# Kernel tuning notes

Measured on AMD Instinct MI355X. Metric: run time of the kernel, lower is better.

Reference implementation:

```python
import jax, jax.numpy as jnp
import numpy as np
from jax import lax

B_, L_ = 2, 512
D_MODEL, EXPAND, HEAD_DIM, NGROUPS, D_STATE, D_CONV = 512, 2, 64, 1, 64, 3
D_INNER = EXPAND * D_MODEL            # 1024
NHEADS = D_INNER // HEAD_DIM          # 16
CONV_DIM = D_INNER + 2 * NGROUPS * D_STATE   # 1152
D_IN_PROJ = 2 * D_INNER + 2 * NGROUPS * D_STATE + NHEADS  # 2192
RMS_EPS = 1e-5


def silu(x):
    return x * jax.nn.sigmoid(x)


def segsum(x):
    # x: (..., T) -> (..., T, T); out[..., i, j] = sum_{j<k<=i} x[..., k], -inf above diag
    T = x.shape[-1]
    xr = jnp.broadcast_to(x[..., None], x.shape + (T,))
    keep = jnp.tril(jnp.ones((T, T), dtype=bool), -1)
    xr = jnp.where(keep, xr, 0.0)
    s = jnp.cumsum(xr, axis=-2)
    diag = jnp.tril(jnp.ones((T, T), dtype=bool), 0)
    return jnp.where(diag, s, -jnp.inf)


def ssd(x, A, Bm, Cm, chunk):
    # x: (b,l,h,p), A: (b,l,h), Bm/Cm: (b,l,g,n); chunk==1 as in the source forward
    b, l, h, p = x.shape
    c = l // chunk
    n = Bm.shape[-1]
    x = x.reshape(b, c, chunk, h, p)
    Bm = Bm.reshape(b, c, chunk, Bm.shape[2], n)
    Cm = Cm.reshape(b, c, chunk, Cm.shape[2], n)
    A = A.reshape(b, c, chunk, h).transpose(0, 3, 1, 2)        # (b,h,c,l)
    A_cumsum = jnp.cumsum(A, axis=-1)
    Lmat = jnp.exp(segsum(A))                                   # (b,h,c,l,l)
    # broadcast group dim (g==1) to heads, matching torch.einsum broadcasting
    Bb = jnp.broadcast_to(Bm, (b, c, chunk, h, n))
    Cb = jnp.broadcast_to(Cm, (b, c, chunk, h, n))
    Y_diag = jnp.einsum('bclhn,bcshn,bhcls,bcshp->bclhp', Cb, Bb, Lmat, x)
    decay_states = jnp.exp(A_cumsum[:, :, :, -1:] - A_cumsum)   # (b,h,c,l)
    states = jnp.einsum('bclhn,bhcl,bclhp->bchpn', Bb, decay_states, x)
    states = jnp.concatenate([jnp.zeros_like(states[:, :1]), states], axis=1)  # (b,c+1,h,p,n)
    A_last = jnp.pad(A_cumsum[:, :, :, -1], ((0, 0), (0, 0), (1, 0)))          # (b,h,c+1)
    decay_chunk = jnp.exp(segsum(A_last))                       # (b,h,c+1,c+1)
    new_states = jnp.einsum('bhzc,bchpn->bzhpn', decay_chunk, states)
    states = new_states[:, :-1]                                 # (b,c,h,p,n)
    state_decay_out = jnp.exp(A_cumsum)
    Y_off = jnp.einsum('bclhn,bchpn,bhcl->bclhp', Cb, states, state_decay_out)
    return (Y_diag + Y_off).reshape(b, l, h, p)


def causal_dwconv(x, w, bias):
    # x: (B,L,C); w: (C,K) depthwise; torch pads (K-1) both sides then slices [:L] == left-pad only
    xt = x.transpose(0, 2, 1)
    y = lax.conv_general_dilated(xt, w[:, None, :], (1,), [(D_CONV - 1, 0)],
                                 feature_group_count=CONV_DIM,
                                 dimension_numbers=('NCH', 'OIH', 'NCH'))
    return y.transpose(0, 2, 1) + bias


def setup_inputs() -> dict:
    key = jax.random.key(0)
    ks = jax.random.split(key, 8)
    u = jax.random.normal(ks[0], (B_, L_, D_MODEL), dtype=jnp.float32)
    W_in = jax.random.normal(ks[1], (D_MODEL, D_IN_PROJ), dtype=jnp.float32) / np.sqrt(D_MODEL).astype(np.float32)
    conv_w = jax.random.normal(ks[2], (CONV_DIM, D_CONV), dtype=jnp.float32) * 0.3
    conv_b = jnp.zeros((CONV_DIM,), dtype=jnp.float32)
    dt = jnp.exp(jax.random.uniform(ks[3], (NHEADS,), dtype=jnp.float32)
                 * (np.float32(np.log(0.1)) - np.float32(np.log(0.001))) + np.float32(np.log(0.001)))
    dt = jnp.clip(dt, 1e-4, None)
    dt_bias = dt + jnp.log(-jnp.expm1(-dt))
    A_log = jnp.log(jax.random.uniform(ks[4], (NHEADS,), dtype=jnp.float32, minval=1.0, maxval=16.0))
    D_param = jnp.ones((NHEADS,), dtype=jnp.float32)
    rms_w = jnp.ones((D_INNER,), dtype=jnp.float32)
    W_out = jax.random.normal(ks[5], (D_INNER, D_MODEL), dtype=jnp.float32) / np.sqrt(D_INNER).astype(np.float32)
    return {"u": u, "W_in": W_in, "conv_w": conv_w, "conv_b": conv_b, "dt_bias": dt_bias,
            "A_log": A_log, "D_param": D_param, "rms_w": rms_w, "W_out": W_out}


def reference(u, W_in, conv_w, conv_b, dt_bias, A_log, D_param, rms_w, W_out):
    b, l, _ = u.shape
    zxbcdt = u @ W_in                                   # (b,l,D_IN_PROJ)
    z = zxbcdt[..., :D_INNER]
    xBC = zxbcdt[..., D_INNER:D_INNER + CONV_DIM]
    dt = zxbcdt[..., D_INNER + CONV_DIM:]
    dt = jax.nn.softplus(dt + dt_bias)                  # (b,l,h)
    A = -jnp.exp(A_log)                                 # (h,)
    xBC = silu(causal_dwconv(xBC, conv_w, conv_b))      # (b,l,CONV_DIM)
    x = xBC[..., :D_INNER].reshape(b, l, NHEADS, HEAD_DIM)
    Bm = xBC[..., D_INNER:D_INNER + D_STATE][:, :, None, :]     # (b,l,1,n)
    Cm = xBC[..., D_INNER + D_STATE:][:, :, None, :]            # (b,l,1,n)
    y = ssd(x * dt[..., None], A * dt, Bm, Cm, 1)       # (b,l,h,p)
    y = y + x * D_param[:, None]
    y = y.reshape(b, l, D_INNER)
    # gated RMSNorm
    yz = y * silu(z)
    y = yz * lax.rsqrt(jnp.mean(yz * yz, axis=-1, keepdims=True) + RMS_EPS) * rms_w
    return y @ W_out
```

## Files before the change

### kernel.cpp

```cpp
#include <hip/hip_runtime.h>
#include <hip/hip_bf16.h>

#define B_SZ 2
#define L_SZ 512
#define D_MODEL 512
#define D_INNER 1024
#define HEAD_DIM 64
#define NHEADS 16
#define D_STATE 64
#define D_CONV 3
#define CONV_DIM 1152
#define D_IN_PROJ 2192
#define BL (B_SZ * L_SZ)
#define RMS_EPS 1e-5f
#define QC 64
#define NCH 8
#define NPAD1 2304
#define PB 72

typedef __attribute__((ext_vector_type(8))) short short8t;
typedef __attribute__((ext_vector_type(8))) unsigned short ushort8t;
typedef __attribute__((ext_vector_type(4))) unsigned short ushort4t;
typedef __attribute__((ext_vector_type(4))) float f32x4;

__device__ __forceinline__ unsigned short f2bf(float f) {
    unsigned u = __float_as_uint(f);
    u += 0x7fff + ((u >> 16) & 1);
    return (unsigned short)(u >> 16);
}
__device__ __forceinline__ float bf2f(unsigned short u) {
    return __uint_as_float(((unsigned)u) << 16);
}

__device__ __forceinline__ void gload_lds16(const void* g, void* lds) {
    __builtin_amdgcn_global_load_lds(
        (const __attribute__((address_space(1))) unsigned int*)g,
        (__attribute__((address_space(3))) unsigned int*)lds, 16, 0, 0);
}

__device__ __forceinline__ void transpose_tile_bf16(const float* __restrict__ src,
                                                    unsigned short* __restrict__ dst,
                                                    int K, int Nin, int tile, int ntn) {
    __shared__ float T[64][65];
    int tid = threadIdx.x;
    int nt = tile % ntn, kt = tile / ntn;
    int n0 = nt * 64, k0 = kt * 64;
#pragma unroll
    for (int rr = 0; rr < 4; ++rr) {
        int k = k0 + (tid >> 4) + rr * 16;
        int nn = (tid & 15) * 4;
#pragma unroll
        for (int q = 0; q < 4; ++q) {
            int n = n0 + nn + q;
            T[(tid >> 4) + rr * 16][nn + q] = (n < Nin) ? src[(size_t)k * Nin + n] : 0.f;
        }
    }
    __syncthreads();
    int nn2 = tid >> 2, kc = tid & 3;
    unsigned short ov[16];
#pragma unroll
    for (int j = 0; j < 16; ++j) ov[j] = f2bf(T[kc * 16 + j][nn2]);
    unsigned short* p = dst + (size_t)(n0 + nn2) * K + k0 + kc * 16;
    *(ushort8t*)p = *(ushort8t*)&ov[0];
    *(ushort8t*)(p + 8) = *(ushort8t*)&ov[8];
}

__global__ __launch_bounds__(256) void prep_kernel(const float* __restrict__ W_in,
                                                   const float* __restrict__ W_out,
                                                   const float* __restrict__ u,
                                                   unsigned short* __restrict__ Wt1,
                                                   unsigned short* __restrict__ Wt2,
                                                   unsigned short* __restrict__ u_bf) {
    int bid = blockIdx.x;
    if (bid < 288) {
        transpose_tile_bf16(W_in, Wt1, D_MODEL, D_IN_PROJ, bid, 36);
    } else if (bid < 416) {
        transpose_tile_bf16(W_out, Wt2, D_INNER, D_MODEL, bid - 288, 8);
    } else {
        int i = ((bid - 416) * 256 + threadIdx.x) * 8;
        float4 v0 = *(const float4*)(u + i);
        float4 v1 = *(const float4*)(u + i + 4);
        unsigned short ov[8] = {f2bf(v0.x), f2bf(v0.y), f2bf(v0.z), f2bf(v0.w),
                                f2bf(v1.x), f2bf(v1.y), f2bf(v1.z), f2bf(v1.w)};
        *(ushort8t*)(u_bf + i) = *(ushort8t*)&ov[0];
    }
}

__global__ __launch_bounds__(256) void gemm_in(const unsigned short* __restrict__ A,
                                               const unsigned short* __restrict__ Bt,
                                               float* __restrict__ C,
                                               unsigned short* __restrict__ xbc,
                                               float* __restrict__ dtb) {
    const int K = D_MODEL;
    __shared__ char sm[49152];
    int tid = threadIdx.x;
    int w = tid >> 6, l = tid & 63;
    int m0 = blockIdx.y * 64, n0 = blockIdx.x * 64;
    int wm = w >> 1, wn = w & 1;

    f32x4 acc[2][2];
#pragma unroll
    for (int i = 0; i < 2; ++i)
#pragma unroll
        for (int j = 0; j < 2; ++j) acc[i][j] = (f32x4){0.f, 0.f, 0.f, 0.f};

    auto stage = [&](const unsigned short* src, int row0, int k0, char* dst) {
#pragma unroll
        for (int p = 0; p < 2; ++p) {
            int c = w * 2 + p;
            int row = c * 8 + (l >> 3);
            int scb = ((l & 7) << 4) ^ ((row & 7) << 4);
            gload_lds16(src + (size_t)(row0 + row) * K + k0 + (scb >> 1), dst + c * 1024);
        }
    };

    const int nkt = K / 64;
    stage(A, m0, 0, sm);
    stage(Bt, n0, 0, sm + 8192);
    stage(A, m0, 64, sm + 16384);
    stage(Bt, n0, 64, sm + 16384 + 8192);

    for (int kt = 0; kt < nkt; ++kt) {
        if (kt + 2 < nkt) {
            char* d = sm + ((kt + 2) % 3) * 16384;
            stage(A, m0, (kt + 2) * 64, d);
            stage(Bt, n0, (kt + 2) * 64, d + 8192);
        }
        int inflight = nkt - 1 - kt;
        if (inflight >= 2)      asm volatile("s_waitcnt vmcnt(8)" ::: "memory");
        else if (inflight == 1) asm volatile("s_waitcnt vmcnt(4)" ::: "memory");
        else                    asm volatile("s_waitcnt vmcnt(0)" ::: "memory");
        __builtin_amdgcn_s_barrier();

        const char* Ab = sm + (kt % 3) * 16384;
        const char* Bb = Ab + 8192;
#pragma unroll
        for (int kk = 0; kk < 2; ++kk) {
            short8t af[2], bf[2];
#pragma unroll
            for (int i = 0; i < 2; ++i) {
                int r = wm * 32 + i * 16 + (l & 15);
                int cb = (kk * 64 + (l >> 4) * 16) ^ ((r & 7) << 4);
                af[i] = *(const short8t*)(Ab + r * 128 + cb);
            }
#pragma unroll
            for (int j = 0; j < 2; ++j) {
                int r = wn * 32 + j * 16 + (l & 15);
                int cb = (kk * 64 + (l >> 4) * 16) ^ ((r & 7) << 4);
                bf[j] = *(const short8t*)(Bb + r * 128 + cb);
            }
#pragma unroll
            for (int i = 0; i < 2; ++i)
#pragma unroll
                for (int j = 0; j < 2; ++j)
                    acc[i][j] = __builtin_amdgcn_mfma_f32_16x16x32_bf16(af[i], bf[j], acc[i][j], 0, 0, 0);
        }
        __builtin_amdgcn_s_barrier();
    }

#pragma unroll
    for (int i = 0; i < 2; ++i)
#pragma unroll
        for (int j = 0; j < 2; ++j) {
            int row = m0 + wm * 32 + i * 16 + (l >> 4) * 4;
            int col = n0 + wn * 32 + j * 16 + (l & 15);
#pragma unroll
            for (int r = 0; r < 4; ++r) {
                float v = acc[i][j][r];
                int rr = row + r;
                if (col < D_INNER) {
                    C[(size_t)rr * D_IN_PROJ + col] = v;
                } else if (col < D_INNER + CONV_DIM) {
                    xbc[(size_t)rr * CONV_DIM + (col - D_INNER)] = f2bf(v);
                } else if (col < D_IN_PROJ) {
                    dtb[(size_t)rr * 16 + (col - D_INNER - CONV_DIM)] = v;
                }
            }
        }
}

__global__ __launch_bounds__(256) void gemm_mfma32(const unsigned short* __restrict__ A,
                                                   const unsigned short* __restrict__ Bt,
                                                   float* __restrict__ C,
                                                   int N, int K) {
    __shared__ char sm[36864];
    int tid = threadIdx.x;
    int w = tid >> 6, l = tid & 63;
    int m0 = blockIdx.y * 32, n0 = blockIdx.x * 64;
    int wm = w >> 1, wn = w & 1;

    f32x4 acc[2];
    acc[0] = (f32x4){0.f, 0.f, 0.f, 0.f};
    acc[1] = (f32x4){0.f, 0.f, 0.f, 0.f};

    auto stageA = [&](int k0, char* dst) {
        int row = w * 8 + (l >> 3);
        int scb = ((l & 7) << 4) ^ ((row & 7) << 4);
        gload_lds16(A + (size_t)(m0 + row) * K + k0 + (scb >> 1), dst + w * 1024);
    };
    auto stageB = [&](int k0, char* dst) {
#pragma unroll
        for (int p = 0; p < 2; ++p) {
            int c = w * 2 + p;
            int row = c * 8 + (l >> 3);
            int scb = ((l & 7) << 4) ^ ((row & 7) << 4);
            gload_lds16(Bt + (size_t)(n0 + row) * K + k0 + (scb >> 1), dst + c * 1024);
        }
    };

    int nkt = K / 64;
    stageA(0, sm); stageB(0, sm + 4096);
    stageA(64, sm + 12288); stageB(64, sm + 12288 + 4096);

    for (int kt = 0; kt < nkt; ++kt) {
        if (kt + 2 < nkt) {
            char* d = sm + ((kt + 2) % 3) * 12288;
            stageA((kt + 2) * 64, d);
            stageB((kt + 2) * 64, d + 4096);
        }
        int inflight = nkt - 1 - kt;
        if (inflight >= 2)      asm volatile("s_waitcnt vmcnt(6)" ::: "memory");
        else if (inflight == 1) asm volatile("s_waitcnt vmcnt(3)" ::: "memory");
        else                    asm volatile("s_waitcnt vmcnt(0)" ::: "memory");
        __builtin_amdgcn_s_barrier();

        const char* Ab = sm + (kt % 3) * 12288;
        const char* Bb = Ab + 4096;
#pragma unroll
        for (int kk = 0; kk < 2; ++kk) {
            short8t af;
            {
                int r = wm * 16 + (l & 15);
                int cb = (kk * 64 + (l >> 4) * 16) ^ ((r & 7) << 4);
                af = *(const short8t*)(Ab + r * 128 + cb);
            }
#pragma unroll
            for (int j = 0; j < 2; ++j) {
                int r = wn * 32 + j * 16 + (l & 15);
                int cb = (kk * 64 + (l >> 4) * 16) ^ ((r & 7) << 4);
                short8t bfv = *(const short8t*)(Bb + r * 128 + cb);
                acc[j] = __builtin_amdgcn_mfma_f32_16x16x32_bf16(af, bfv, acc[j], 0, 0, 0);
            }
        }
        __builtin_amdgcn_s_barrier();
    }

#pragma unroll
    for (int j = 0; j < 2; ++j) {
        int col = n0 + wn * 32 + j * 16 + (l & 15);
        int rowb = m0 + wm * 16 + (l >> 4) * 4;
#pragma unroll
        for (int r = 0; r < 4; ++r)
            C[(size_t)(rowb + r) * N + col] = acc[j][r];
    }
}

__device__ __forceinline__ float4 conv4b(const unsigned short* __restrict__ xrow,
                                         int gl, int ch,
                                         const float* __restrict__ conv_w,
                                         const float* __restrict__ conv_b) {
    ushort4t u2 = *(const ushort4t*)(xrow + ch);
    ushort4t u1 = {0, 0, 0, 0}, u0 = {0, 0, 0, 0};
    if (gl >= 1) u1 = *(const ushort4t*)(xrow + ch - CONV_DIM);
    if (gl >= 2) u0 = *(const ushort4t*)(xrow + ch - 2 * CONV_DIM);
    float4 o;
    float a;
    a = conv_b[ch+0] + conv_w[(ch+0)*3]*bf2f(u0[0]) + conv_w[(ch+0)*3+1]*bf2f(u1[0]) + conv_w[(ch+0)*3+2]*bf2f(u2[0]);
    o.x = a / (1.f + __expf(-a));
    a = conv_b[ch+1] + conv_w[(ch+1)*3]*bf2f(u0[1]) + conv_w[(ch+1)*3+1]*bf2f(u1[1]) + conv_w[(ch+1)*3+2]*bf2f(u2[1]);
    o.y = a / (1.f + __expf(-a));
    a = conv_b[ch+2] + conv_w[(ch+2)*3]*bf2f(u0[2]) + conv_w[(ch+2)*3+1]*bf2f(u1[2]) + conv_w[(ch+2)*3+2]*bf2f(u2[2]);
    o.z = a / (1.f + __expf(-a));
    a = conv_b[ch+3] + conv_w[(ch+3)*3]*bf2f(u0[3]) + conv_w[(ch+3)*3+1]*bf2f(u1[3]) + conv_w[(ch+3)*3+2]*bf2f(u2[3]);
    o.w = a / (1.f + __expf(-a));
    return o;
}

__global__ __launch_bounds__(256) void ssd_passA(const unsigned short* __restrict__ xbc,
                                                 const float* __restrict__ dtb,
                                                 const float* __restrict__ conv_w,
                                                 const float* __restrict__ conv_b,
                                                 const float* __restrict__ dt_bias,
                                                 const float* __restrict__ A_log,
                                                 const float* __restrict__ D_param,
                                                 float* __restrict__ y,
                                                 float* __restrict__ Zbuf,
                                                 float* __restrict__ Ebuf) {
    int blk = blockIdx.x;
    int h = blk & 15;
    int c = (blk >> 4) & 7;
    int b = blk >> 7;
    int tid = threadIdx.x;

    __shared__ __align__(16) unsigned short Cs_bf[QC][PB];
    __shared__ __align__(16) unsigned short Bs_bf[QC][PB];
    __shared__ __align__(16) unsigned short XDT_bf[QC][PB];
    __shared__ __align__(16) unsigned short BTw_bf[QC][PB];
    __shared__ float csh[QC], dts[QC], wh[QC];
#define PS_bf Cs_bf

    int bl0 = b * L_SZ + c * QC;

    if (tid < 64) {
        int t = tid;
        float draw = dtb[(size_t)(bl0 + t) * 16 + h];
        float dtv = draw + dt_bias[h];
        dtv = (dtv > 20.f) ? dtv : log1pf(expf(dtv));
        float A = -expf(A_log[h]);
        float cs = A * dtv;
#pragma unroll
        for (int off = 1; off < 64; off <<= 1) {
            float tmp = __shfl_up(cs, off);
            if (t >= off) cs += tmp;
        }
        float cs63 = __shfl(cs, 63);
        dts[t] = dtv;
        csh[t] = cs;
        wh[t] = __expf(cs63 - cs);
        Ebuf[(((size_t)(b * NHEADS + h) * NCH) + c) * QC + t] = __expf(cs);
    }

    int row16 = tid >> 4;
    int col4 = (tid & 15) * 4;
#pragma unroll
    for (int r = 0; r < 4; ++r) {
        int t = r * 16 + row16;
        int gl = c * QC + t;
        const unsigned short* xrow = xbc + (size_t)(bl0 + t) * CONV_DIM;
        float4 Bv = conv4b(xrow, gl, D_INNER + col4, conv_w, conv_b);
        float4 Cv = conv4b(xrow, gl, D_INNER + D_STATE + col4, conv_w, conv_b);
        ushort4t bq = {f2bf(Bv.x), f2bf(Bv.y), f2bf(Bv.z), f2bf(Bv.w)};
        ushort4t cq = {f2bf(Cv.x), f2bf(Cv.y), f2bf(Cv.z), f2bf(Cv.w)};
        *(ushort4t*)&Bs_bf[t][col4] = bq;
        *(ushort4t*)&Cs_bf[t][col4] = cq;
    }
    __syncthreads();

#pragma unroll
    for (int r = 0; r < 4; ++r) {
        int t = r * 16 + row16;
        int gl = c * QC + t;
        const unsigned short* xrow = xbc + (size_t)(bl0 + t) * CONV_DIM;
        float4 xv = conv4b(xrow, gl, h * HEAD_DIM + col4, conv_w, conv_b);
        float d = dts[t], wt = wh[t];
        xv.x *= d; xv.y *= d; xv.z *= d; xv.w *= d;
        ushort4t xq = {f2bf(xv.x), f2bf(xv.y), f2bf(xv.z), f2bf(xv.w)};
        ushort4t bq = *(ushort4t*)&Bs_bf[t][col4];
#pragma unroll
        for (int q = 0; q < 4; ++q) {
            XDT_bf[col4 + q][t] = xq[q];
            BTw_bf[col4 + q][t] = f2bf(bf2f(bq[q]) * wt);
        }
    }
    __syncthreads();

    int l = tid & 63, wv = tid >> 6;
    int wm = wv >> 1, wn = wv & 1;
    int fr = l & 15, fq = l >> 4;

    f32x4 g[2][2];
    {
#pragma unroll
        for (int i = 0; i < 2; ++i)
#pragma unroll
            for (int j = 0; j < 2; ++j) g[i][j] = (f32x4){0.f, 0.f, 0.f, 0.f};
#pragma unroll
        for (int kk = 0; kk < 2; ++kk) {
            short8t af[2], bb[2];
#pragma unroll
            for (int i = 0; i < 2; ++i)
                af[i] = *(const short8t*)&Cs_bf[wm * 32 + i * 16 + fr][kk * 32 + fq * 8];
#pragma unroll
            for (int j = 0; j < 2; ++j)
                bb[j] = *(const short8t*)&Bs_bf[wn * 32 + j * 16 + fr][kk * 32 + fq * 8];
#pragma unroll
            for (int i = 0; i < 2; ++i)
#pragma unroll
                for (int j = 0; j < 2; ++j)
                    g[i][j] = __builtin_amdgcn_mfma_f32_16x16x32_bf16(af[i], bb[j], g[i][j], 0, 0, 0);
        }
    }
    __syncthreads();

    {
#pragma unroll
        for (int i = 0; i < 2; ++i)
#pragma unroll
            for (int j = 0; j < 2; ++j) {
                int s = wn * 32 + j * 16 + fr;
                float css = csh[s];
#pragma unroll
                for (int r = 0; r < 4; ++r) {
                    int t = wm * 32 + i * 16 + fq * 4 + r;
                    float v = (s <= t) ? g[i][j][r] * __expf(csh[t] - css) : 0.f;
                    PS_bf[t][s] = f2bf(v);
                }
            }
    }
    __syncthreads();

    {
        f32x4 yv[2][2];
#pragma unroll
        for (int i = 0; i < 2; ++i)
#pragma unroll
            for (int j = 0; j < 2; ++j) yv[i][j] = (f32x4){0.f, 0.f, 0.f, 0.f};
#pragma unroll
        for (int kk = 0; kk < 2; ++kk) {
            short8t af[2], bb[2];
#pragma unroll
            for (int i = 0; i < 2; ++i)
                af[i] = *(const short8t*)&PS_bf[wm * 32 + i * 16 + fr][kk * 32 + fq * 8];
#pragma unroll
            for (int j = 0; j < 2; ++j)
                bb[j] = *(const short8t*)&XDT_bf[wn * 32 + j * 16 + fr][kk * 32 + fq * 8];
#pragma unroll
            for (int i = 0; i < 2; ++i)
#pragma unroll
                for (int j = 0; j < 2; ++j)
                    yv[i][j] = __builtin_amdgcn_mfma_f32_16x16x32_bf16(af[i], bb[j], yv[i][j], 0, 0, 0);
        }
        float Dp = D_param[h];
#pragma unroll
        for (int i = 0; i < 2; ++i)
#pragma unroll
            for (int j = 0; j < 2; ++j) {
                int p = wn * 32 + j * 16 + fr;
#pragma unroll
                for (int r = 0; r < 4; ++r) {
                    int t = wm * 32 + i * 16 + fq * 4 + r;
                    float xval = bf2f(XDT_bf[p][t]);
                    float fct = Dp / dts[t];
                    y[(size_t)(bl0 + t) * D_INNER + h * HEAD_DIM + p] =
                        yv[i][j][r] + fct * xval;
                }
            }
    }

    {
        f32x4 zv[2][2];
#pragma unroll
        for (int i = 0; i < 2; ++i)
#pragma unroll
            for (int j = 0; j < 2; ++j) zv[i][j] = (f32x4){0.f, 0.f, 0.f, 0.f};
#pragma unroll
        for (int kk = 0; kk < 2; ++kk) {
            short8t af[2], bb[2];
#pragma unroll
            for (int i = 0; i < 2; ++i)
                af[i] = *(const short8t*)&XDT_bf[wm * 32 + i * 16 + fr][kk * 32 + fq * 8];
#pragma unroll
            for (int j = 0; j < 2; ++j)
                bb[j] = *(const short8t*)&BTw_bf[wn * 32 + j * 16 + fr][kk * 32 + fq * 8];
#pragma unroll
            for (int i = 0; i < 2; ++i)
#pragma unroll
                for (int j = 0; j < 2; ++j)
                    zv[i][j] = __builtin_amdgcn_mfma_f32_16x16x32_bf16(af[i], bb[j], zv[i][j], 0, 0, 0);
        }
        float* Zr = Zbuf + (((size_t)(b * NHEADS + h) * NCH) + c) * (HEAD_DIM * D_STATE);
#pragma unroll
        for (int i = 0; i < 2; ++i)
#pragma unroll
            for (int j = 0; j < 2; ++j) {
                int n = wn * 32 + j * 16 + fr;
#pragma unroll
                for (int r = 0; r < 4; ++r) {
                    int p = wm * 32 + i * 16 + fq * 4 + r;
                    Zr[p * D_STATE + n] = zv[i][j][r];
                }
            }
    }
#undef PS_bf
}

__global__ __launch_bounds__(256) void ssd_passC(const unsigned short* __restrict__ xbc,
                                                 const float* __restrict__ conv_w,
                                                 const float* __restrict__ conv_b,
                                                 const float* __restrict__ Zbuf,
                                                 const float* __restrict__ Ebuf,
                                                 float* __restrict__ y) {
    int blk = blockIdx.x;
    int h = blk & 15;
    int q = blk >> 4;
    int c = 1 + (q % 7);
    int b = q / 7;
    int tid = threadIdx.x;

    __shared__ __align__(16) unsigned short Cs_bf[QC][PB];
    __shared__ __align__(16) unsigned short S_bf[QC][PB];
    __shared__ float Eh[QC];

    int bl0 = b * L_SZ + c * QC;
    const float* Zb = Zbuf + ((size_t)(b * NHEADS + h) * NCH) * (HEAD_DIM * D_STATE);
    const float* Eb = Ebuf + ((size_t)(b * NHEADS + h) * NCH) * QC;

    {
        int p = tid >> 2, nq = (tid & 3) * 16;
        float S16[16];
#pragma unroll
        for (int qq = 0; qq < 16; ++qq) S16[qq] = 0.f;
        float wgt = 1.f;
        for (int j = c - 1; j >= 0; --j) {
            const float* Zj = Zb + (size_t)j * (HEAD_DIM * D_STATE) + p * D_STATE + nq;
#pragma unroll
            for (int q4 = 0; q4 < 4; ++q4) {
                float4 z = *(const float4*)(Zj + q4 * 4);
                S16[q4 * 4 + 0] += wgt * z.x;
                S16[q4 * 4 + 1] += wgt * z.y;
                S16[q4 * 4 + 2] += wgt * z.z;
                S16[q4 * 4 + 3] += wgt * z.w;
            }
            wgt *= Eb[(size_t)j * QC + 63];
        }
#pragma unroll
        for (int q4 = 0; q4 < 4; ++q4) {
            ushort4t s4 = {f2bf(S16[q4 * 4 + 0]), f2bf(S16[q4 * 4 + 1]),
                           f2bf(S16[q4 * 4 + 2]), f2bf(S16[q4 * 4 + 3])};
            *(ushort4t*)&S_bf[p][nq + q4 * 4] = s4;
        }
    }

    int row16 = tid >> 4, col4 = (tid & 15) * 4;
#pragma unroll
    for (int r = 0; r < 4; ++r) {
        int t = r * 16 + row16;
        int gl = c * QC + t;
        const unsigned short* xrow = xbc + (size_t)(bl0 + t) * CONV_DIM;
        float4 Cv = conv4b(xrow, gl, D_INNER + D_STATE + col4, conv_w, conv_b);
        ushort4t cq = {f2bf(Cv.x), f2bf(Cv.y), f2bf(Cv.z), f2bf(Cv.w)};
        *(ushort4t*)&Cs_bf[t][col4] = cq;
    }
    if (tid < 64)
        Eh[tid] = Ebuf[(((size_t)(b * NHEADS + h) * NCH) + c) * QC + tid];
    __syncthreads();

    int l = tid & 63, wv = tid >> 6;
    int wm = wv >> 1, wn = wv & 1;
    int fr = l & 15, fq = l >> 4;
    f32x4 acc[2][2];
#pragma unroll
    for (int i = 0; i < 2; ++i)
#pragma unroll
        for (int j = 0; j < 2; ++j) acc[i][j] = (f32x4){0.f, 0.f, 0.f, 0.f};
#pragma unroll
    for (int kk = 0; kk < 2; ++kk) {
        short8t af[2], bb[2];
#pragma unroll
        for (int i = 0; i < 2; ++i)
            af[i] = *(const short8t*)&Cs_bf[wm * 32 + i * 16 + fr][kk * 32 + fq * 8];
#pragma unroll
        for (int j = 0; j < 2; ++j)
            bb[j] = *(const short8t*)&S_bf[wn * 32 + j * 16 + fr][kk * 32 + fq * 8];
#pragma unroll
        for (int i = 0; i < 2; ++i)
#pragma unroll
            for (int j = 0; j < 2; ++j)
                acc[i][j] = __builtin_amdgcn_mfma_f32_16x16x32_bf16(af[i], bb[j], acc[i][j], 0, 0, 0);
    }
#pragma unroll
    for (int i = 0; i < 2; ++i)
#pragma unroll
        for (int j = 0; j < 2; ++j) {
            int p = wn * 32 + j * 16 + fr;
#pragma unroll
            for (int r = 0; r < 4; ++r) {
                int t = wm * 32 + i * 16 + fq * 4 + r;
                float* yp = y + (size_t)(bl0 + t) * D_INNER + h * HEAD_DIM + p;
                *yp += Eh[t] * acc[i][j][r];
            }
        }
}

__global__ __launch_bounds__(256) void gated_rmsnorm_kernel(const float* __restrict__ zxbcdt,
                                                            const float* __restrict__ y,
                                                            const float* __restrict__ rms_w,
                                                            unsigned short* __restrict__ yn_bf) {
    int bl = blockIdx.x;
    int tid = threadIdx.x;
    __shared__ float red[4];
    __shared__ float sscale;
    float vals[4];
    float sumsq = 0.f;
#pragma unroll
    for (int i = 0; i < 4; ++i) {
        int col = tid + i * 256;
        float yv = y[(size_t)bl * D_INNER + col];
        float z = zxbcdt[(size_t)bl * D_IN_PROJ + col];
        float yz = yv * (z / (1.f + expf(-z)));
        vals[i] = yz;
        sumsq += yz * yz;
    }
#pragma unroll
    for (int off = 32; off; off >>= 1) sumsq += __shfl_xor(sumsq, off);
    int wave = tid >> 6, lane = tid & 63;
    if (lane == 0) red[wave] = sumsq;
    __syncthreads();
    if (tid == 0) {
        float t = red[0] + red[1] + red[2] + red[3];
        sscale = rsqrtf(t / (float)D_INNER + RMS_EPS);
    }
    __syncthreads();
    float sc = sscale;
#pragma unroll
    for (int i = 0; i < 4; ++i) {
        int col = tid + i * 256;
        yn_bf[(size_t)bl * D_INNER + col] = f2bf(vals[i] * sc * rms_w[col]);
    }
}

extern "C" void kernel_launch(void* const* d_in, const int* in_sizes, int n_in,
                              void* d_out, int out_size, void* d_ws, size_t ws_size,
                              hipStream_t stream) {
    const float* u       = (const float*)d_in[0];
    const float* W_in    = (const float*)d_in[1];
    const float* conv_w  = (const float*)d_in[2];
    const float* conv_b  = (const float*)d_in[3];
    const float* dt_bias = (const float*)d_in[4];
    const float* A_log   = (const float*)d_in[5];
    const float* D_param = (const float*)d_in[6];
    const float* rms_w   = (const float*)d_in[7];
    const float* W_out   = (const float*)d_in[8];
    float* out = (float*)d_out;

    float* ws = (float*)d_ws;
    float* zxbcdt = ws;
    float* y      = zxbcdt + (size_t)BL * D_IN_PROJ;
    float* Zbuf   = y + (size_t)BL * D_INNER;
    float* Ebuf   = Zbuf + (size_t)32 * NCH * 4096;
    float* dtb    = Ebuf + (size_t)32 * NCH * QC;
    unsigned short* u_bf  = (unsigned short*)(dtb + (size_t)BL * 16);
    unsigned short* Wt1   = u_bf + (size_t)BL * D_MODEL;
    unsigned short* Wt2   = Wt1 + (size_t)NPAD1 * D_MODEL;
    unsigned short* yn_bf = Wt2 + (size_t)D_MODEL * D_INNER;
    unsigned short* xbc   = yn_bf + (size_t)BL * D_INNER;

    prep_kernel<<<672, 256, 0, stream>>>(W_in, W_out, u, Wt1, Wt2, u_bf);

    gemm_in<<<dim3(NPAD1 / 64, BL / 64), 256, 0, stream>>>(
        u_bf, Wt1, zxbcdt, xbc, dtb);

    ssd_passA<<<B_SZ * NCH * NHEADS, 256, 0, stream>>>(
        xbc, dtb, conv_w, conv_b, dt_bias, A_log, D_param, y, Zbuf, Ebuf);
    ssd_passC<<<224, 256, 0, stream>>>(
        xbc, conv_w, conv_b, Zbuf, Ebuf, y);

    gated_rmsnorm_kernel<<<BL, 256, 0, stream>>>(zxbcdt, y, rms_w, yn_bf);

    gemm_mfma32<<<dim3(D_MODEL / 64, BL / 32), 256, 0, stream>>>(
        yn_bf, Wt2, out, D_MODEL, D_INNER);
}
```

Measured before the change: 46.97 us.

## Hoist conv+SiLU and softplus into a separate kernel; stage SSD tiles via LDS DMA

Moves the causal depthwise conv, SiLU and dt softplus out of the SSD chunk kernels into a dedicated per-row kernel that writes bf16 activations once. The chunk kernels then load B, C and X tiles with direct global-to-LDS loads into swizzled layouts, and XOR-swizzled transposed buffers replace the padded ones. This removes the conv work that was repeated for B and C across 16 heads and for C in pass C. The cost is an extra launch and an extra round trip of the conv output through global memory.

```diff
diff --git a/kernel.cpp b/kernel.cpp
--- a/kernel.cpp
+++ b/kernel.cpp
@@ -16,7 +16,6 @@
 #define QC 64
 #define NCH 8
 #define NPAD1 2304
-#define PB 72
 
 typedef __attribute__((ext_vector_type(8))) short short8t;
 typedef __attribute__((ext_vector_type(8))) unsigned short ushort8t;
@@ -177,82 +176,6 @@
                 }
             }
         }
-}
-
-__global__ __launch_bounds__(256) void gemm_mfma32(const unsigned short* __restrict__ A,
-                                                   const unsigned short* __restrict__ Bt,
-                                                   float* __restrict__ C,
-                                                   int N, int K) {
-    __shared__ char sm[36864];
-    int tid = threadIdx.x;
-    int w = tid >> 6, l = tid & 63;
-    int m0 = blockIdx.y * 32, n0 = blockIdx.x * 64;
-    int wm = w >> 1, wn = w & 1;
-
-    f32x4 acc[2];
-    acc[0] = (f32x4){0.f, 0.f, 0.f, 0.f};
-    acc[1] = (f32x4){0.f, 0.f, 0.f, 0.f};
-
-    auto stageA = [&](int k0, char* dst) {
-        int row = w * 8 + (l >> 3);
-        int scb = ((l & 7) << 4) ^ ((row & 7) << 4);
-        gload_lds16(A + (size_t)(m0 + row) * K + k0 + (scb >> 1), dst + w * 1024);
-    };
-    auto stageB = [&](int k0, char* dst) {
-#pragma unroll
-        for (int p = 0; p < 2; ++p) {
-            int c = w * 2 + p;
-            int row = c * 8 + (l >> 3);
-            int scb = ((l & 7) << 4) ^ ((row & 7) << 4);
-            gload_lds16(Bt + (size_t)(n0 + row) * K + k0 + (scb >> 1), dst + c * 1024);
-        }
-    };
-
-    int nkt = K / 64;
-    stageA(0, sm); stageB(0, sm + 4096);
-    stageA(64, sm + 12288); stageB(64, sm + 12288 + 4096);
-
-    for (int kt = 0; kt < nkt; ++kt) {
-        if (kt + 2 < nkt) {
-            char* d = sm + ((kt + 2) % 3) * 12288;
-            stageA((kt + 2) * 64, d);
-            stageB((kt + 2) * 64, d + 4096);
-        }
-        int inflight = nkt - 1 - kt;
-        if (inflight >= 2)      asm volatile("s_waitcnt vmcnt(6)" ::: "memory");
-        else if (inflight == 1) asm volatile("s_waitcnt vmcnt(3)" ::: "memory");
-        else                    asm volatile("s_waitcnt vmcnt(0)" ::: "memory");
-        __builtin_amdgcn_s_barrier();
-
-        const char* Ab = sm + (kt % 3) * 12288;
-        const char* Bb = Ab + 4096;
-#pragma unroll
-        for (int kk = 0; kk < 2; ++kk) {
-            short8t af;
-            {
-                int r = wm * 16 + (l & 15);
-                int cb = (kk * 64 + (l >> 4) * 16) ^ ((r & 7) << 4);
-                af = *(const short8t*)(Ab + r * 128 + cb);
-            }
-#pragma unroll
-            for (int j = 0; j < 2; ++j) {
-                int r = wn * 32 + j * 16 + (l & 15);
-                int cb = (kk * 64 + (l >> 4) * 16) ^ ((r & 7) << 4);
-                short8t bfv = *(const short8t*)(Bb + r * 128 + cb);
-                acc[j] = __builtin_amdgcn_mfma_f32_16x16x32_bf16(af, bfv, acc[j], 0, 0, 0);
-            }
-        }
-        __builtin_amdgcn_s_barrier();
-    }
-
-#pragma unroll
-    for (int j = 0; j < 2; ++j) {
-        int col = n0 + wn * 32 + j * 16 + (l & 15);
-        int rowb = m0 + wm * 16 + (l >> 4) * 4;
-#pragma unroll
-        for (int r = 0; r < 4; ++r)
-            C[(size_t)(rowb + r) * N + col] = acc[j][r];
-    }
 }
 
 __device__ __forceinline__ float4 conv4b(const unsigned short* __restrict__ xrow,
@@ -276,11 +199,30 @@
     return o;
 }
 
-__global__ __launch_bounds__(256) void ssd_passA(const unsigned short* __restrict__ xbc,
-                                                 const float* __restrict__ dtb,
-                                                 const float* __restrict__ conv_w,
-                                                 const float* __restrict__ conv_b,
-                                                 const float* __restrict__ dt_bias,
+__global__ __launch_bounds__(256) void conv_silu_kernel(const unsigned short* __restrict__ xbc,
+                                                        const float* __restrict__ conv_w,
+                                                        const float* __restrict__ conv_b,
+                                                        const float* __restrict__ dtb,
+                                                        const float* __restrict__ dt_bias,
+                                                        unsigned short* __restrict__ xc,
+                                                        float* __restrict__ dtp) {
+    int bl = blockIdx.x;
+    int gl = bl & (L_SZ - 1);
+    int tid = threadIdx.x;
+    const unsigned short* xrow = xbc + (size_t)bl * CONV_DIM;
+    for (int ch = tid * 4; ch < CONV_DIM; ch += 1024) {
+        float4 o = conv4b(xrow, gl, ch, conv_w, conv_b);
+        ushort4t q = {f2bf(o.x), f2bf(o.y), f2bf(o.z), f2bf(o.w)};
+        *(ushort4t*)(xc + (size_t)bl * CONV_DIM + ch) = q;
+    }
+    if (tid < 16) {
+        float d = dtb[(size_t)bl * 16 + tid] + dt_bias[tid];
+        dtp[(size_t)bl * 16 + tid] = (d > 20.f) ? d : log1pf(expf(d));
+    }
+}
+
+__global__ __launch_bounds__(256) void ssd_passA(const unsigned short* __restrict__ xc,
+                                                 const float* __restrict__ dtp,
                                                  const float* __restrict__ A_log,
                                                  const float* __restrict__ D_param,
                                                  float* __restrict__ y,
@@ -291,21 +233,35 @@
     int c = (blk >> 4) & 7;
     int b = blk >> 7;
     int tid = threadIdx.x;
-
-    __shared__ __align__(16) unsigned short Cs_bf[QC][PB];
-    __shared__ __align__(16) unsigned short Bs_bf[QC][PB];
-    __shared__ __align__(16) unsigned short XDT_bf[QC][PB];
-    __shared__ __align__(16) unsigned short BTw_bf[QC][PB];
+    int w = tid >> 6, l = tid & 63;
+
+    __shared__ __align__(16) unsigned short Bs[64 * 64];
+    __shared__ __align__(16) unsigned short Cs[64 * 64];
+    __shared__ __align__(16) unsigned short Xs[64 * 64];
+    __shared__ __align__(16) unsigned short XDT[64 * 72];
+    __shared__ __align__(16) unsigned short BTw[64 * 72];
+    __shared__ __align__(16) unsigned short P[64 * 72];
     __shared__ float csh[QC], dts[QC], wh[QC];
-#define PS_bf Cs_bf
 
     int bl0 = b * L_SZ + c * QC;
+    const unsigned short* xbase = xc + (size_t)bl0 * CONV_DIM;
+
+    auto stageT = [&](const unsigned short* src, unsigned short* dst) {
+#pragma unroll
+        for (int p = 0; p < 2; ++p) {
+            int cc = w * 2 + p;
+            int row = cc * 8 + (l >> 3);
+            int scb = ((l & 7) << 4) ^ ((row & 7) << 4);
+            gload_lds16(src + (size_t)row * CONV_DIM + (scb >> 1), (char*)dst + cc * 1024);
+        }
+    };
+    stageT(xbase + D_INNER, Bs);
+    stageT(xbase + D_INNER + D_STATE, Cs);
+    stageT(xbase + h * HEAD_DIM, Xs);
 
     if (tid < 64) {
         int t = tid;
-        float draw = dtb[(size_t)(bl0 + t) * 16 + h];
-        float dtv = draw + dt_bias[h];
-        dtv = (dtv > 20.f) ? dtv : log1pf(expf(dtv));
+        float dtv = dtp[(size_t)(bl0 + t) * 16 + h];
         float A = -expf(A_log[h]);
         float cs = A * dtv;
 #pragma unroll
@@ -319,43 +275,29 @@
         wh[t] = __expf(cs63 - cs);
         Ebuf[(((size_t)(b * NHEADS + h) * NCH) + c) * QC + t] = __expf(cs);
     }
+    asm volatile("s_waitcnt vmcnt(0)" ::: "memory");
+    __syncthreads();
 
     int row16 = tid >> 4;
     int col4 = (tid & 15) * 4;
 #pragma unroll
     for (int r = 0; r < 4; ++r) {
         int t = r * 16 + row16;
-        int gl = c * QC + t;
-        const unsigned short* xrow = xbc + (size_t)(bl0 + t) * CONV_DIM;
-        float4 Bv = conv4b(xrow, gl, D_INNER + col4, conv_w, conv_b);
-        float4 Cv = conv4b(xrow, gl, D_INNER + D_STATE + col4, conv_w, conv_b);
-        ushort4t bq = {f2bf(Bv.x), f2bf(Bv.y), f2bf(Bv.z), f2bf(Bv.w)};
-        ushort4t cq = {f2bf(Cv.x), f2bf(Cv.y), f2bf(Cv.z), f2bf(Cv.w)};
-        *(ushort4t*)&Bs_bf[t][col4] = bq;
-        *(ushort4t*)&Cs_bf[t][col4] = cq;
+        int xoff = (col4 * 2) ^ ((t & 7) << 4);
+        ushort4t xq = *(const ushort4t*)((const char*)Xs + t * 128 + xoff);
+        ushort4t bq = *(const ushort4t*)((const char*)Bs + t * 128 + xoff);
+        float d = dts[t], wt = wh[t];
+#pragma unroll
+        for (int q = 0; q < 4; ++q) {
+            int ch = col4 + q;
+            int f8 = ((ch >> 2) & 7) << 3;
+            XDT[ch * 72 + (t ^ f8)] = f2bf(bf2f(xq[q]) * d);
+            BTw[ch * 72 + (t ^ f8)] = f2bf(bf2f(bq[q]) * wt);
+        }
     }
     __syncthreads();
 
-#pragma unroll
-    for (int r = 0; r < 4; ++r) {
-        int t = r * 16 + row16;
-        int gl = c * QC + t;
-        const unsigned short* xrow = xbc + (size_t)(bl0 + t) * CONV_DIM;
-        float4 xv = conv4b(xrow, gl, h * HEAD_DIM + col4, conv_w, conv_b);
-        float d = dts[t], wt = wh[t];
-        xv.x *= d; xv.y *= d; xv.z *= d; xv.w *= d;
-        ushort4t xq = {f2bf(xv.x), f2bf(xv.y), f2bf(xv.z), f2bf(xv.w)};
-        ushort4t bq = *(ushort4t*)&Bs_bf[t][col4];
-#pragma unroll
-        for (int q = 0; q < 4; ++q) {
-            XDT_bf[col4 + q][t] = xq[q];
-            BTw_bf[col4 + q][t] = f2bf(bf2f(bq[q]) * wt);
-        }
-    }
-    __syncthreads();
-
-    int l = tid & 63, wv = tid >> 6;
-    int wm = wv >> 1, wn = wv & 1;
+    int wm = w >> 1, wn = w & 1;
     int fr = l & 15, fq = l >> 4;
 
     f32x4 g[2][2];
@@ -368,11 +310,17 @@
         for (int kk = 0; kk < 2; ++kk) {
             short8t af[2], bb[2];
 #pragma unroll
-            for (int i = 0; i < 2; ++i)
-                af[i] = *(const short8t*)&Cs_bf[wm * 32 + i * 16 + fr][kk * 32 + fq * 8];
-#pragma unroll
-            for (int j = 0; j < 2; ++j)
-                bb[j] = *(const short8t*)&Bs_bf[wn * 32 + j * 16 + fr][kk * 32 + fq * 8];
+            for (int i = 0; i < 2; ++i) {
+                int r = wm * 32 + i * 16 + fr;
+                int cb = (kk * 64 + fq * 16) ^ ((r & 7) << 4);
+                af[i] = *(const short8t*)((const char*)Cs + r * 128 + cb);
+            }
+#pragma unroll
+            for (int j = 0; j < 2; ++j) {
+                int r = wn * 32 + j * 16 + fr;
+                int cb = (kk * 64 + fq * 16) ^ ((r & 7) << 4);
+                bb[j] = *(const short8t*)((const char*)Bs + r * 128 + cb);
+            }
 #pragma unroll
             for (int i = 0; i < 2; ++i)
 #pragma unroll
@@ -380,7 +328,6 @@
                     g[i][j] = __builtin_amdgcn_mfma_f32_16x16x32_bf16(af[i], bb[j], g[i][j], 0, 0, 0);
         }
     }
-    __syncthreads();
 
     {
 #pragma unroll
@@ -393,7 +340,7 @@
                 for (int r = 0; r < 4; ++r) {
                     int t = wm * 32 + i * 16 + fq * 4 + r;
                     float v = (s <= t) ? g[i][j][r] * __expf(csh[t] - css) : 0.f;
-                    PS_bf[t][s] = f2bf(v);
+                    P[t * 72 + s] = f2bf(v);
                 }
             }
     }
@@ -408,12 +355,15 @@
 #pragma unroll
         for (int kk = 0; kk < 2; ++kk) {
             short8t af[2], bb[2];
+            int K0 = kk * 32 + fq * 8;
 #pragma unroll
             for (int i = 0; i < 2; ++i)
-                af[i] = *(const short8t*)&PS_bf[wm * 32 + i * 16 + fr][kk * 32 + fq * 8];
-#pragma unroll
-            for (int j = 0; j < 2; ++j)
-                bb[j] = *(const short8t*)&XDT_bf[wn * 32 + j * 16 + fr][kk * 32 + fq * 8];
+                af[i] = *(const short8t*)&P[(wm * 32 + i * 16 + fr) * 72 + K0];
+#pragma unroll
+            for (int j = 0; j < 2; ++j) {
+                int r = wn * 32 + j * 16 + fr;
+                bb[j] = *(const short8t*)&XDT[r * 72 + (K0 ^ (((r >> 2) & 7) << 3))];
+            }
 #pragma unroll
             for (int i = 0; i < 2; ++i)
 #pragma unroll
@@ -426,10 +376,11 @@
 #pragma unroll
             for (int j = 0; j < 2; ++j) {
                 int p = wn * 32 + j * 16 + fr;
+                int f8 = ((p >> 2) & 7) << 3;
 #pragma unroll
                 for (int r = 0; r < 4; ++r) {
                     int t = wm * 32 + i * 16 + fq * 4 + r;
-                    float xval = bf2f(XDT_bf[p][t]);
+                    float xval = bf2f(XDT[p * 72 + (t ^ f8)]);
                     float fct = Dp / dts[t];
                     y[(size_t)(bl0 + t) * D_INNER + h * HEAD_DIM + p] =
                         yv[i][j][r] + fct * xval;
@@ -446,12 +397,17 @@
 #pragma unroll
         for (int kk = 0; kk < 2; ++kk) {
             short8t af[2], bb[2];
-#pragma unroll
-            for (int i = 0; i < 2; ++i)
-                af[i] = *(const short8t*)&XDT_bf[wm * 32 + i * 16 + fr][kk * 32 + fq * 8];
-#pragma unroll
-            for (int j = 0; j < 2; ++j)
-                bb[j] = *(const short8t*)&BTw_bf[wn * 32 + j * 16 + fr][kk * 32 + fq * 8];
+            int K0 = kk * 32 + fq * 8;
+#pragma unroll
+            for (int i = 0; i < 2; ++i) {
+                int r = wm * 32 + i * 16 + fr;
+                af[i] = *(const short8t*)&XDT[r * 72 + (K0 ^ (((r >> 2) & 7) << 3))];
+            }
+#pragma unroll
+            for (int j = 0; j < 2; ++j) {
+                int r = wn * 32 + j * 16 + fr;
+                bb[j] = *(const short8t*)&BTw[r * 72 + (K0 ^ (((r >> 2) & 7) << 3))];
+            }
 #pragma unroll
             for (int i = 0; i < 2; ++i)
 #pragma unroll
@@ -471,12 +427,9 @@
                 }
             }
     }
-#undef PS_bf
-}
-
-__global__ __launch_bounds__(256) void ssd_passC(const unsigned short* __restrict__ xbc,
-                                                 const float* __restrict__ conv_w,
-                                                 const float* __restrict__ conv_b,
+}
+
+__global__ __launch_bounds__(256) void ssd_passC(const unsigned short* __restrict__ xc,
                                                  const float* __restrict__ Zbuf,
                                                  const float* __restrict__ Ebuf,
                                                  float* __restrict__ y) {
@@ -486,14 +439,26 @@
     int c = 1 + (q % 7);
     int b = q / 7;
     int tid = threadIdx.x;
-
-    __shared__ __align__(16) unsigned short Cs_bf[QC][PB];
-    __shared__ __align__(16) unsigned short S_bf[QC][PB];
+    int w = tid >> 6, l = tid & 63;
+
+    __shared__ __align__(16) unsigned short Cs[64 * 64];
+    __shared__ __align__(16) unsigned short S_bf[64 * 72];
     __shared__ float Eh[QC];
 
     int bl0 = b * L_SZ + c * QC;
+    const unsigned short* xbase = xc + (size_t)bl0 * CONV_DIM + D_INNER + D_STATE;
     const float* Zb = Zbuf + ((size_t)(b * NHEADS + h) * NCH) * (HEAD_DIM * D_STATE);
     const float* Eb = Ebuf + ((size_t)(b * NHEADS + h) * NCH) * QC;
+
+    {
+#pragma unroll
+        for (int p = 0; p < 2; ++p) {
+            int cc = w * 2 + p;
+            int row = cc * 8 + (l >> 3);
+            int scb = ((l & 7) << 4) ^ ((row & 7) << 4);
+            gload_lds16(xbase + (size_t)row * CONV_DIM + (scb >> 1), (char*)Cs + cc * 1024);
+        }
+    }
 
     {
         int p = tid >> 2, nq = (tid & 3) * 16;
@@ -517,26 +482,15 @@
         for (int q4 = 0; q4 < 4; ++q4) {
             ushort4t s4 = {f2bf(S16[q4 * 4 + 0]), f2bf(S16[q4 * 4 + 1]),
                            f2bf(S16[q4 * 4 + 2]), f2bf(S16[q4 * 4 + 3])};
-            *(ushort4t*)&S_bf[p][nq + q4 * 4] = s4;
-        }
-    }
-
-    int row16 = tid >> 4, col4 = (tid & 15) * 4;
-#pragma unroll
-    for (int r = 0; r < 4; ++r) {
-        int t = r * 16 + row16;
-        int gl = c * QC + t;
-        const unsigned short* xrow = xbc + (size_t)(bl0 + t) * CONV_DIM;
-        float4 Cv = conv4b(xrow, gl, D_INNER + D_STATE + col4, conv_w, conv_b);
-        ushort4t cq = {f2bf(Cv.x), f2bf(Cv.y), f2bf(Cv.z), f2bf(Cv.w)};
-        *(ushort4t*)&Cs_bf[t][col4] = cq;
+            *(ushort4t*)&S_bf[p * 72 + nq + q4 * 4] = s4;
+        }
     }
     if (tid < 64)
         Eh[tid] = Ebuf[(((size_t)(b * NHEADS + h) * NCH) + c) * QC + tid];
+    asm volatile("s_waitcnt vmcnt(0)" ::: "memory");
     __syncthreads();
 
-    int l = tid & 63, wv = tid >> 6;
-    int wm = wv >> 1, wn = wv & 1;
+    int wm = w >> 1, wn = w & 1;
     int fr = l & 15, fq = l >> 4;
     f32x4 acc[2][2];
 #pragma unroll
@@ -546,12 +500,16 @@
 #pragma unroll
     for (int kk = 0; kk < 2; ++kk) {
         short8t af[2], bb[2];
-#pragma unroll
-        for (int i = 0; i < 2; ++i)
-            af[i] = *(const short8t*)&Cs_bf[wm * 32 + i * 16 + fr][kk * 32 + fq * 8];
+        int K0 = kk * 32 + fq * 8;
+#pragma unroll
+        for (int i = 0; i < 2; ++i) {
+            int r = wm * 32 + i * 16 + fr;
+            int cb = (kk * 64 + fq * 16) ^ ((r & 7) << 4);
+            af[i] = *(const short8t*)((const char*)Cs + r * 128 + cb);
+        }
 #pragma unroll
         for (int j = 0; j < 2; ++j)
-            bb[j] = *(const short8t*)&S_bf[wn * 32 + j * 16 + fr][kk * 32 + fq * 8];
+            bb[j] = *(const short8t*)&S_bf[(wn * 32 + j * 16 + fr) * 72 + K0];
 #pragma unroll
         for (int i = 0; i < 2; ++i)
 #pragma unroll
@@ -606,6 +564,82 @@
     for (int i = 0; i < 4; ++i) {
         int col = tid + i * 256;
         yn_bf[(size_t)bl * D_INNER + col] = f2bf(vals[i] * sc * rms_w[col]);
+    }
+}
+
+__global__ __launch_bounds__(256) void gemm_mfma32(const unsigned short* __restrict__ A,
+                                                   const unsigned short* __restrict__ Bt,
+                                                   float* __restrict__ C,
+                                                   int N, int K) {
+    __shared__ char sm[36864];
+    int tid = threadIdx.x;
+    int w = tid >> 6, l = tid & 63;
+    int m0 = blockIdx.y * 32, n0 = blockIdx.x * 64;
+    int wm = w >> 1, wn = w & 1;
+
+    f32x4 acc[2];
+    acc[0] = (f32x4){0.f, 0.f, 0.f, 0.f};
+    acc[1] = (f32x4){0.f, 0.f, 0.f, 0.f};
+
+    auto stageA = [&](int k0, char* dst) {
+        int row = w * 8 + (l >> 3);
+        int scb = ((l & 7) << 4) ^ ((row & 7) << 4);
+        gload_lds16(A + (size_t)(m0 + row) * K + k0 + (scb >> 1), dst + w * 1024);
+    };
+    auto stageB = [&](int k0, char* dst) {
+#pragma unroll
+        for (int p = 0; p < 2; ++p) {
+            int c = w * 2 + p;
+            int row = c * 8 + (l >> 3);
+            int scb = ((l & 7) << 4) ^ ((row & 7) << 4);
+            gload_lds16(Bt + (size_t)(n0 + row) * K + k0 + (scb >> 1), dst + c * 1024);
+        }
+    };
+
+    int nkt = K / 64;
+    stageA(0, sm); stageB(0, sm + 4096);
+    stageA(64, sm + 12288); stageB(64, sm + 12288 + 4096);
+
+    for (int kt = 0; kt < nkt; ++kt) {
+        if (kt + 2 < nkt) {
+            char* d = sm + ((kt + 2) % 3) * 12288;
+            stageA((kt + 2) * 64, d);
+            stageB((kt + 2) * 64, d + 4096);
+        }
+        int inflight = nkt - 1 - kt;
+        if (inflight >= 2)      asm volatile("s_waitcnt vmcnt(6)" ::: "memory");
+        else if (inflight == 1) asm volatile("s_waitcnt vmcnt(3)" ::: "memory");
+        else                    asm volatile("s_waitcnt vmcnt(0)" ::: "memory");
+        __builtin_amdgcn_s_barrier();
+
+        const char* Ab = sm + (kt % 3) * 12288;
+        const char* Bb = Ab + 4096;
+#pragma unroll
+        for (int kk = 0; kk < 2; ++kk) {
+            short8t af;
+            {
+                int r = wm * 16 + (l & 15);
+                int cb = (kk * 64 + (l >> 4) * 16) ^ ((r & 7) << 4);
+                af = *(const short8t*)(Ab + r * 128 + cb);
+            }
+#pragma unroll
+            for (int j = 0; j < 2; ++j) {
+                int r = wn * 32 + j * 16 + (l & 15);
+                int cb = (kk * 64 + (l >> 4) * 16) ^ ((r & 7) << 4);
+                short8t bfv = *(const short8t*)(Bb + r * 128 + cb);
+                acc[j] = __builtin_amdgcn_mfma_f32_16x16x32_bf16(af, bfv, acc[j], 0, 0, 0);
+            }
+        }
+        __builtin_amdgcn_s_barrier();
+    }
+
+#pragma unroll
+    for (int j = 0; j < 2; ++j) {
+        int col = n0 + wn * 32 + j * 16 + (l & 15);
+        int rowb = m0 + wm * 16 + (l >> 4) * 4;
+#pragma unroll
+        for (int r = 0; r < 4; ++r)
+            C[(size_t)(rowb + r) * N + col] = acc[j][r];
     }
 }
 
@@ -629,21 +663,24 @@
     float* Zbuf   = y + (size_t)BL * D_INNER;
     float* Ebuf   = Zbuf + (size_t)32 * NCH * 4096;
     float* dtb    = Ebuf + (size_t)32 * NCH * QC;
-    unsigned short* u_bf  = (unsigned short*)(dtb + (size_t)BL * 16);
+    float* dtp    = dtb + (size_t)BL * 16;
+    unsigned short* u_bf  = (unsigned short*)(dtp + (size_t)BL * 16);
     unsigned short* Wt1   = u_bf + (size_t)BL * D_MODEL;
     unsigned short* Wt2   = Wt1 + (size_t)NPAD1 * D_MODEL;
     unsigned short* yn_bf = Wt2 + (size_t)D_MODEL * D_INNER;
     unsigned short* xbc   = yn_bf + (size_t)BL * D_INNER;
+    unsigned short* xc    = xbc + (size_t)BL * CONV_DIM;
 
     prep_kernel<<<672, 256, 0, stream>>>(W_in, W_out, u, Wt1, Wt2, u_bf);
 
     gemm_in<<<dim3(NPAD1 / 64, BL / 64), 256, 0, stream>>>(
         u_bf, Wt1, zxbcdt, xbc, dtb);
 
+    conv_silu_kernel<<<BL, 256, 0, stream>>>(xbc, conv_w, conv_b, dtb, dt_bias, xc, dtp);
+
     ssd_passA<<<B_SZ * NCH * NHEADS, 256, 0, stream>>>(
-        xbc, dtb, conv_w, conv_b, dt_bias, A_log, D_param, y, Zbuf, Ebuf);
-    ssd_passC<<<224, 256, 0, stream>>>(
-        xbc, conv_w, conv_b, Zbuf, Ebuf, y);
+        xc, dtp, A_log, D_param, y, Zbuf, Ebuf);
+    ssd_passC<<<224, 256, 0, stream>>>(xc, Zbuf, Ebuf, y);
 
     gated_rmsnorm_kernel<<<BL, 256, 0, stream>>>(zxbcdt, y, rms_w, yn_bf);
 
```

New measurement: 47.40 us. Within noise of the previous version (+0.9%).
